# Performance work log

Measured on AMD Instinct MI355X. Metric: run time of the kernel, lower is better.

The kernel has to match this reference:

```python
import jax, jax.numpy as jnp
import numpy as np


def setup_inputs() -> dict:
    key = jax.random.key(0)
    k1, k2, k3, k4, k5 = jax.random.split(key, 5)
    B, D, H, W, C = 2, 16, 16, 16, 256
    x = jax.random.normal(k1, (B, D, H, W, C), dtype=jnp.float32)
    Wf = jax.random.normal(k2, (C, C // 4), dtype=jnp.float32) * (1.0 / np.sqrt(C))
    Wg = jax.random.normal(k3, (C, C // 4), dtype=jnp.float32) * (1.0 / np.sqrt(C))
    Wh = jax.random.normal(k4, (C, C), dtype=jnp.float32) * (1.0 / np.sqrt(C))
    gamma = jax.random.normal(k5, (1,), dtype=jnp.float32) * 0.1
    return {"x": x, "Wf": Wf, "Wg": Wg, "Wh": Wh, "gamma": gamma}


def reference(x, Wf, Wg, Wh, gamma):
    B, D, H, W, C = x.shape
    N = D * H * W
    xf = x.reshape(B, N, C)  # hw_flatten of input (1x1x1 conv == per-position matmul)
    f = jnp.einsum('bnc,cf->bnf', xf, Wf)   # [B, N, C//4]
    g = jnp.einsum('bnc,cf->bnf', xf, Wg)   # [B, N, C//4]
    h = jnp.einsum('bnc,cf->bnf', xf, Wh)   # [B, N, C]
    s = jnp.einsum('bnf,bmf->bnm', g, f)    # g @ f^T, [B, N, N]
    beta = jax.nn.softmax(s, axis=-1)
    o = jnp.einsum('bnm,bmc->bnc', beta, h)  # [B, N, C]
    out = gamma * o.reshape(B, D, H, W, C) + x
    beta_out = beta.reshape(-1, D, H, W, 1)  # [B*N, D, H, W, 1] as in original
    return (out, beta_out)
```

## Files before the change

### kernel.cpp

```cpp
#include <hip/hip_runtime.h>

#define NPOS 4096
#define CDIM 256
#define FDIM 64

typedef short short8 __attribute__((ext_vector_type(8)));
typedef float f32x4 __attribute__((ext_vector_type(4)));

__device__ __forceinline__ unsigned short f2bf(float v) {
  unsigned u = __float_as_uint(v);
  unsigned r = (u + 0x7fffu + ((u >> 16) & 1u)) >> 16;
  return (unsigned short)r;
}
__device__ __forceinline__ float bf2f(unsigned short u) {
  return __uint_as_float((unsigned)u << 16);
}
__device__ __forceinline__ short8 as_s8(uint4 u) {
  return *reinterpret_cast<short8*>(&u);
}
__device__ __forceinline__ void gload_lds16(const void* g, void* l) {
  __builtin_amdgcn_global_load_lds(
      (const __attribute__((address_space(1))) unsigned int*)g,
      (__attribute__((address_space(3))) unsigned int*)l, 16, 0, 0);
}

__global__ __launch_bounds__(256) void proj_kernel(
    const float* __restrict__ x, const float* __restrict__ Wf,
    const float* __restrict__ Wg, const float* __restrict__ Wh,
    unsigned short* __restrict__ f_hi, unsigned short* __restrict__ f_lo,
    unsigned short* __restrict__ g_hi, unsigned short* __restrict__ g_lo,
    unsigned short* __restrict__ h_t) {
  __shared__ float xs[16][CDIM];
  const int row0 = blockIdx.x * 16;
  const int t = threadIdx.x;
  {
    const float4* xv = reinterpret_cast<const float4*>(x + (size_t)row0 * CDIM);
    float4* sv = reinterpret_cast<float4*>(&xs[0][0]);
#pragma unroll
    for (int i = 0; i < 4; ++i) sv[t + 256 * i] = xv[t + 256 * i];
  }
  __syncthreads();
  {
    float acc[16];
#pragma unroll
    for (int r = 0; r < 16; ++r) acc[r] = 0.f;
    for (int k = 0; k < CDIM; k += 4) {
      const float w0 = Wh[(size_t)(k + 0) * CDIM + t];
      const float w1 = Wh[(size_t)(k + 1) * CDIM + t];
      const float w2 = Wh[(size_t)(k + 2) * CDIM + t];
      const float w3 = Wh[(size_t)(k + 3) * CDIM + t];
#pragma unroll
      for (int r = 0; r < 16; ++r) {
        const float4 xv = *reinterpret_cast<const float4*>(&xs[r][k]);
        float a = acc[r];
        a = fmaf(xv.x, w0, a);
        a = fmaf(xv.y, w1, a);
        a = fmaf(xv.z, w2, a);
        a = fmaf(xv.w, w3, a);
        acc[r] = a;
      }
    }
    const int b = row0 >> 12;
    const int lr = row0 & (NPOS - 1);
    unsigned wd[8];
#pragma unroll
    for (int i = 0; i < 8; ++i)
      wd[i] = (unsigned)f2bf(acc[2 * i]) | ((unsigned)f2bf(acc[2 * i + 1]) << 16);
    uint4* base = reinterpret_cast<uint4*>(h_t + ((size_t)(b * CDIM + t)) * NPOS);
    const int m = t & 7;
    const int c0 = lr >> 3;
    base[c0 ^ m] = make_uint4(wd[0], wd[1], wd[2], wd[3]);
    base[(c0 + 1) ^ m] = make_uint4(wd[4], wd[5], wd[6], wd[7]);
  }
  {
    const int col = t & 63;
    const int rb = (t >> 6) * 4;
    const int colq = col >> 3, cwi = col & 7;
    float af[4] = {0.f, 0.f, 0.f, 0.f};
    float ag[4] = {0.f, 0.f, 0.f, 0.f};
    for (int k = 0; k < CDIM; k += 4) {
      const float wf0 = Wf[(size_t)(k + 0) * FDIM + col];
      const float wf1 = Wf[(size_t)(k + 1) * FDIM + col];
      const float wf2 = Wf[(size_t)(k + 2) * FDIM + col];
      const float wf3 = Wf[(size_t)(k + 3) * FDIM + col];
      const float wg0 = Wg[(size_t)(k + 0) * FDIM + col];
      const float wg1 = Wg[(size_t)(k + 1) * FDIM + col];
      const float wg2 = Wg[(size_t)(k + 2) * FDIM + col];
      const float wg3 = Wg[(size_t)(k + 3) * FDIM + col];
#pragma unroll
      for (int r = 0; r < 4; ++r) {
        const float4 xv = *reinterpret_cast<const float4*>(&xs[rb + r][k]);
        float a = af[r], bb = ag[r];
        a = fmaf(xv.x, wf0, a); a = fmaf(xv.y, wf1, a);
        a = fmaf(xv.z, wf2, a); a = fmaf(xv.w, wf3, a);
        bb = fmaf(xv.x, wg0, bb); bb = fmaf(xv.y, wg1, bb);
        bb = fmaf(xv.z, wg2, bb); bb = fmaf(xv.w, wg3, bb);
        af[r] = a; ag[r] = bb;
      }
    }
#pragma unroll
    for (int r = 0; r < 4; ++r) {
      const int row = row0 + rb + r;
      const int ph = ((colq ^ (row & 7)) << 3) | cwi;
      const size_t of = (size_t)row * FDIM + ph;
      const size_t og = (size_t)row * FDIM + col;
      const unsigned short fh = f2bf(af[r]);
      const unsigned short gh = f2bf(ag[r]);
      f_hi[of] = fh;
      f_lo[of] = f2bf(af[r] - bf2f(fh));
      g_hi[og] = gh;
      g_lo[og] = f2bf(ag[r] - bf2f(gh));
    }
  }
}

__global__ __launch_bounds__(1024, 4) void attn_fused_kernel(
    const unsigned short* __restrict__ f_hi, const unsigned short* __restrict__ f_lo,
    const unsigned short* __restrict__ g_hi, const unsigned short* __restrict__ g_lo,
    const unsigned short* __restrict__ h_t, const float* __restrict__ x,
    const float* __restrict__ gamma, float* __restrict__ beta,
    float* __restrict__ out) {
  __shared__ __align__(16) char shraw[73728];
  __shared__ float partl[16][16];
  __shared__ float linvs[32];
  uint4 (*Fh)[128][8] = reinterpret_cast<uint4(*)[128][8]>(shraw);
  uint4 (*Fl)[128][8] = reinterpret_cast<uint4(*)[128][8]>(shraw + 32768);
  uint4 (*Ab)[32][8] = reinterpret_cast<uint4(*)[32][8]>(shraw);
  uint4 (*Bb)[256][8] = reinterpret_cast<uint4(*)[256][8]>(shraw + 8192);

  const int wg = blockIdx.x;
  const int wgid = (wg & 7) * 32 + (wg >> 3);
  const int b = wgid >> 7;
  const int row0 = (wgid & 127) * 32;
  const int t = threadIdx.x;
  const int w = t >> 6;
  const int l = t & 63;
  const int lr = l & 15;
  const int lk = l >> 4;

  const int wr = w >> 3;
  const int wq = w & 7;
  const int arow = row0 + wr * 16 + lr;
  short8 gh[2], gl[2];
  {
    const unsigned short* gH = g_hi + ((size_t)(b * NPOS + arow)) * FDIM + lk * 8;
    const unsigned short* gL = g_lo + ((size_t)(b * NPOS + arow)) * FDIM + lk * 8;
#pragma unroll
    for (int ks = 0; ks < 2; ++ks) {
      gh[ks] = *reinterpret_cast<const short8*>(gH + ks * 32);
      gl[ks] = *reinterpret_cast<const short8*>(gL + ks * 32);
    }
  }
  const unsigned short* fbh = f_hi + (size_t)b * NPOS * FDIM;
  const unsigned short* fbl = f_lo + (size_t)b * NPOS * FDIM;
  unsigned short* Pb = (unsigned short*)(beta + (size_t)b * NPOS * NPOS);
  unsigned short* prow = Pb + (size_t)arow * (2 * NPOS) + NPOS;
  const int rsw = lr & 7;
  float lsum = 0.f;
  const int srow_ = t >> 3, sch_ = t & 7;

#define STAGEA(buf, tile)                                                      \
  do {                                                                         \
    const int tr_ = (tile) * 128 + srow_;                                      \
    gload_lds16(fbh + (size_t)tr_ * FDIM + sch_ * 8,                           \
                (char*)&Fh[buf][0][0] + (size_t)t * 16);                       \
    gload_lds16(fbl + (size_t)tr_ * FDIM + sch_ * 8,                           \
                (char*)&Fl[buf][0][0] + (size_t)t * 16);                       \
  } while (0)

  STAGEA(0, 0);
  asm volatile("s_waitcnt vmcnt(0) lgkmcnt(0)\ns_barrier" ::: "memory");

  const int rrA = wq * 16 + lr;
  const int fsw = rrA & 7;
  int buf = 0;
  for (int tile = 0; tile < 32; ++tile) {
    if (tile < 31) STAGEA(buf ^ 1, tile + 1);
    __builtin_amdgcn_sched_barrier(0);
    const uint4 h0 = Fh[buf][rrA][lk ^ fsw];
    const uint4 h1 = Fh[buf][rrA][(lk + 4) ^ fsw];
    const uint4 q0 = Fl[buf][rrA][lk ^ fsw];
    const uint4 q1 = Fl[buf][rrA][(lk + 4) ^ fsw];
    f32x4 acca = {0.f, 0.f, 0.f, 0.f};
    f32x4 accb = {0.f, 0.f, 0.f, 0.f};
    acca = __builtin_amdgcn_mfma_f32_16x16x32_bf16(as_s8(h0), gh[0], acca, 0, 0, 0);
    accb = __builtin_amdgcn_mfma_f32_16x16x32_bf16(as_s8(h0), gl[0], accb, 0, 0, 0);
    acca = __builtin_amdgcn_mfma_f32_16x16x32_bf16(as_s8(q0), gh[0], acca, 0, 0, 0);
    accb = __builtin_amdgcn_mfma_f32_16x16x32_bf16(as_s8(h1), gh[1], accb, 0, 0, 0);
    acca = __builtin_amdgcn_mfma_f32_16x16x32_bf16(as_s8(q1), gh[1], acca, 0, 0, 0);
    accb = __builtin_amdgcn_mfma_f32_16x16x32_bf16(as_s8(h1), gl[1], accb, 0, 0, 0);
    const f32x4 acc = acca + accb;
    const int cq = tile * 128 + wq * 16 + lk * 4;
    const float e0 = __expf(acc[0]);
    const float e1 = __expf(acc[1]);
    const float e2 = __expf(acc[2]);
    const float e3 = __expf(acc[3]);
    lsum += (e0 + e1) + (e2 + e3);
    uint2 pk;
    pk.x = (unsigned)f2bf(e0) | ((unsigned)f2bf(e1) << 16);
    pk.y = (unsigned)f2bf(e2) | ((unsigned)f2bf(e3) << 16);
    const int sidx = (((cq >> 3) ^ rsw) << 3) | (cq & 7);
    *reinterpret_cast<uint2*>(prow + sidx) = pk;
    asm volatile("s_waitcnt vmcnt(1) lgkmcnt(0)\ns_barrier" ::: "memory");
    buf ^= 1;
  }
#undef STAGEA

  lsum += __shfl_xor(lsum, 16);
  lsum += __shfl_xor(lsum, 32);
  if (l < 16) partl[w][l] = lsum;
  __syncthreads();
  if (t < 32) {
    const int half = t >> 4;
    float s = 0.f;
#pragma unroll
    for (int q = 0; q < 8; ++q) s += partl[half * 8 + q][t & 15];
    linvs[t] = __frcp_rn(s);
  }
  asm volatile("s_waitcnt vmcnt(0) lgkmcnt(0)\ns_barrier" ::: "memory");

  const size_t hoff = (size_t)b * CDIM * NPOS;
  const unsigned short* Pub = (const unsigned short*)(beta + (size_t)b * NPOS * NPOS);

#define STAGEB(buf, kt)                                                         \
  do {                                                                          \
    {                                                                           \
      const int slot_ = w * 128 + l;                                            \
      const unsigned short* g_ = h_t + hoff + (size_t)(slot_ >> 3) * NPOS +     \
                                 (size_t)((kt) * 8 + (slot_ & 7)) * 8;          \
      gload_lds16(g_, (unsigned short*)&Bb[buf][0][0] + (size_t)(w * 128) * 8); \
    }                                                                           \
    {                                                                           \
      const int slot_ = w * 128 + 64 + l;                                       \
      const unsigned short* g_ = h_t + hoff + (size_t)(slot_ >> 3) * NPOS +     \
                                 (size_t)((kt) * 8 + (slot_ & 7)) * 8;          \
      gload_lds16(g_, (unsigned short*)&Bb[buf][0][0] +                         \
                          (size_t)(w * 128 + 64) * 8);                          \
    }                                                                           \
    if (t < 256) {                                                              \
      const unsigned short* g_ = Pub + (size_t)(row0 + (t >> 3)) * (2 * NPOS) + \
                                 NPOS + (size_t)((kt) * 8 + (t & 7)) * 8;       \
      gload_lds16(g_, (unsigned short*)&Ab[buf][0][0] + (size_t)(w * 64) * 8);  \
    }                                                                           \
  } while (0)

  f32x4 acc0 = {0.f, 0.f, 0.f, 0.f}, acc1 = {0.f, 0.f, 0.f, 0.f};
  const int wrB = w & 1;
  const int wcB = w >> 1;
  const int arB = wrB * 16 + lr;
  const int c0 = wcB * 32 + lr;
  const int c1 = c0 + 16;
  const int brow = t >> 5;
  const int jj = t & 31;

  STAGEB(0, 0);
  asm volatile("s_waitcnt vmcnt(0) lgkmcnt(0)\ns_barrier" ::: "memory");

  buf = 0;
  for (int kt = 0; kt < 64; ++kt) {
    if (kt < 63) STAGEB(buf ^ 1, kt + 1);
    __builtin_amdgcn_sched_barrier(0);
    {
      const uint4 a0 = Ab[buf][arB][lk ^ (arB & 7)];
      const uint4 a1 = Ab[buf][arB][(4 + lk) ^ (arB & 7)];
      const uint4 b00 = Bb[buf][c0][lk ^ (c0 & 7)];
      const uint4 b01 = Bb[buf][c1][lk ^ (c1 & 7)];
      const uint4 b10 = Bb[buf][c0][(4 + lk) ^ (c0 & 7)];
      const uint4 b11 = Bb[buf][c1][(4 + lk) ^ (c1 & 7)];
      acc0 = __builtin_amdgcn_mfma_f32_16x16x32_bf16(as_s8(a0), as_s8(b00), acc0, 0, 0, 0);
      acc1 = __builtin_amdgcn_mfma_f32_16x16x32_bf16(as_s8(a0), as_s8(b01), acc1, 0, 0, 0);
      acc0 = __builtin_amdgcn_mfma_f32_16x16x32_bf16(as_s8(a1), as_s8(b10), acc0, 0, 0, 0);
      acc1 = __builtin_amdgcn_mfma_f32_16x16x32_bf16(as_s8(a1), as_s8(b11), acc1, 0, 0, 0);
    }
    {
      const float il = linvs[brow];
      const unsigned* arow_ = reinterpret_cast<const unsigned*>(&Ab[buf][brow][0]);
      const unsigned u = arow_[(((jj >> 2) ^ (brow & 7)) << 2) | (jj & 3)];
      float2 v;
      v.x = bf2f((unsigned short)(u & 0xffffu)) * il;
      v.y = bf2f((unsigned short)(u >> 16)) * il;
      *reinterpret_cast<float2*>(beta + (size_t)(b * NPOS + row0 + brow) * NPOS +
                                 (size_t)kt * 64 + jj * 2) = v;
    }
    asm volatile("s_waitcnt vmcnt(1) lgkmcnt(0)\ns_barrier" ::: "memory");
    buf ^= 1;
  }
#undef STAGEB

  const float gam = gamma[0];
#pragma unroll
  for (int r = 0; r < 4; ++r) {
    const int lrr = wrB * 16 + lk * 4 + r;
    const int orow = row0 + lrr;
    const float sc = gam * linvs[lrr];
    const size_t i0 = ((size_t)b * NPOS + orow) * CDIM + wcB * 32 + lr;
    out[i0] = fmaf(sc, acc0[r], x[i0]);
    out[i0 + 16] = fmaf(sc, acc1[r], x[i0 + 16]);
  }
}

extern "C" void kernel_launch(void* const* d_in, const int* in_sizes, int n_in,
                              void* d_out, int out_size, void* d_ws, size_t ws_size,
                              hipStream_t stream) {
  (void)in_sizes; (void)n_in; (void)out_size; (void)ws_size;
  const float* x = (const float*)d_in[0];
  const float* Wf = (const float*)d_in[1];
  const float* Wg = (const float*)d_in[2];
  const float* Wh = (const float*)d_in[3];
  const float* gamma = (const float*)d_in[4];

  float* out = (float*)d_out;
  float* beta = out + (size_t)2 * NPOS * CDIM;

  unsigned short* h_t = (unsigned short*)d_ws;
  unsigned short* f_hi = h_t + (size_t)2 * CDIM * NPOS;
  unsigned short* f_lo = f_hi + (size_t)2 * NPOS * FDIM;
  unsigned short* g_hi = f_lo + (size_t)2 * NPOS * FDIM;
  unsigned short* g_lo = g_hi + (size_t)2 * NPOS * FDIM;

  hipLaunchKernelGGL(proj_kernel, dim3(2 * NPOS / 16), dim3(256), 0, stream,
                     x, Wf, Wg, Wh, f_hi, f_lo, g_hi, g_lo, h_t);
  hipLaunchKernelGGL(attn_fused_kernel, dim3(256), dim3(1024), 0, stream,
                     f_hi, f_lo, g_hi, g_lo, h_t, x, gamma, beta, out);
}
```

Before: 133.0 us.

## Halve rows per workgroup to launch 512 blocks of 512 threads

The fused attention kernel now handles 16 query rows per workgroup with 8 waves instead of 32 rows with 16 waves, doubling the grid to 512 workgroups. The staging loops, wave-to-tile mapping, LDS layout and the remapping of workgroups to batch and row are all adjusted to match. The aim is better spread across the MI355X compute units and less barrier cost per workgroup. In exchange, each F tile and each h tile staged into LDS now serves half as many rows, so global and LDS traffic per unit of work roughly doubles.

```diff
diff --git a/kernel.cpp b/kernel.cpp
--- a/kernel.cpp
+++ b/kernel.cpp
@@ -114,33 +114,31 @@
   }
 }
 
-__global__ __launch_bounds__(1024, 4) void attn_fused_kernel(
+__global__ __launch_bounds__(512, 4) void attn_fused_kernel(
     const unsigned short* __restrict__ f_hi, const unsigned short* __restrict__ f_lo,
     const unsigned short* __restrict__ g_hi, const unsigned short* __restrict__ g_lo,
     const unsigned short* __restrict__ h_t, const float* __restrict__ x,
     const float* __restrict__ gamma, float* __restrict__ beta,
     float* __restrict__ out) {
-  __shared__ __align__(16) char shraw[73728];
-  __shared__ float partl[16][16];
-  __shared__ float linvs[32];
+  __shared__ __align__(16) char shraw[69632];
+  __shared__ float partl[8][16];
+  __shared__ float linvs[16];
   uint4 (*Fh)[128][8] = reinterpret_cast<uint4(*)[128][8]>(shraw);
   uint4 (*Fl)[128][8] = reinterpret_cast<uint4(*)[128][8]>(shraw + 32768);
-  uint4 (*Ab)[32][8] = reinterpret_cast<uint4(*)[32][8]>(shraw);
-  uint4 (*Bb)[256][8] = reinterpret_cast<uint4(*)[256][8]>(shraw + 8192);
+  uint4 (*Ab)[16][8] = reinterpret_cast<uint4(*)[16][8]>(shraw);
+  uint4 (*Bb)[256][8] = reinterpret_cast<uint4(*)[256][8]>(shraw + 4096);
 
   const int wg = blockIdx.x;
-  const int wgid = (wg & 7) * 32 + (wg >> 3);
-  const int b = wgid >> 7;
-  const int row0 = (wgid & 127) * 32;
+  const int wgid = (wg & 7) * 64 + (wg >> 3);
+  const int b = wgid >> 8;
+  const int row0 = (wgid & 255) * 16;
   const int t = threadIdx.x;
   const int w = t >> 6;
   const int l = t & 63;
   const int lr = l & 15;
   const int lk = l >> 4;
 
-  const int wr = w >> 3;
-  const int wq = w & 7;
-  const int arow = row0 + wr * 16 + lr;
+  const int arow = row0 + lr;
   short8 gh[2], gl[2];
   {
     const unsigned short* gH = g_hi + ((size_t)(b * NPOS + arow)) * FDIM + lk * 8;
@@ -157,21 +155,25 @@
   unsigned short* prow = Pb + (size_t)arow * (2 * NPOS) + NPOS;
   const int rsw = lr & 7;
   float lsum = 0.f;
-  const int srow_ = t >> 3, sch_ = t & 7;
 
 #define STAGEA(buf, tile)                                                      \
   do {                                                                         \
-    const int tr_ = (tile) * 128 + srow_;                                      \
-    gload_lds16(fbh + (size_t)tr_ * FDIM + sch_ * 8,                           \
-                (char*)&Fh[buf][0][0] + (size_t)t * 16);                       \
-    gload_lds16(fbl + (size_t)tr_ * FDIM + sch_ * 8,                           \
-                (char*)&Fl[buf][0][0] + (size_t)t * 16);                       \
+    const int tile0_ = (tile) * 128;                                           \
+    _Pragma("unroll")                                                          \
+    for (int j = 0; j < 2; ++j) {                                              \
+      const int slot_ = j * 512 + t;                                           \
+      const int row_ = slot_ >> 3, ch_ = slot_ & 7;                            \
+      gload_lds16(fbh + (size_t)(tile0_ + row_) * FDIM + ch_ * 8,              \
+                  (char*)&Fh[buf][0][0] + (size_t)slot_ * 16);                 \
+      gload_lds16(fbl + (size_t)(tile0_ + row_) * FDIM + ch_ * 8,              \
+                  (char*)&Fl[buf][0][0] + (size_t)slot_ * 16);                 \
+    }                                                                          \
   } while (0)
 
   STAGEA(0, 0);
   asm volatile("s_waitcnt vmcnt(0) lgkmcnt(0)\ns_barrier" ::: "memory");
 
-  const int rrA = wq * 16 + lr;
+  const int rrA = w * 16 + lr;
   const int fsw = rrA & 7;
   int buf = 0;
   for (int tile = 0; tile < 32; ++tile) {
@@ -190,7 +192,7 @@
     acca = __builtin_amdgcn_mfma_f32_16x16x32_bf16(as_s8(q1), gh[1], acca, 0, 0, 0);
     accb = __builtin_amdgcn_mfma_f32_16x16x32_bf16(as_s8(h1), gl[1], accb, 0, 0, 0);
     const f32x4 acc = acca + accb;
-    const int cq = tile * 128 + wq * 16 + lk * 4;
+    const int cq = tile * 128 + w * 16 + lk * 4;
     const float e0 = __expf(acc[0]);
     const float e1 = __expf(acc[1]);
     const float e2 = __expf(acc[2]);
@@ -210,11 +212,10 @@
   lsum += __shfl_xor(lsum, 32);
   if (l < 16) partl[w][l] = lsum;
   __syncthreads();
-  if (t < 32) {
-    const int half = t >> 4;
+  if (t < 16) {
     float s = 0.f;
 #pragma unroll
-    for (int q = 0; q < 8; ++q) s += partl[half * 8 + q][t & 15];
+    for (int q = 0; q < 8; ++q) s += partl[q][t];
     linvs[t] = __frcp_rn(s);
   }
   asm volatile("s_waitcnt vmcnt(0) lgkmcnt(0)\ns_barrier" ::: "memory");
@@ -224,31 +225,22 @@
 
 #define STAGEB(buf, kt)                                                         \
   do {                                                                          \
-    {                                                                           \
-      const int slot_ = w * 128 + l;                                            \
+    _Pragma("unroll")                                                           \
+    for (int j = 0; j < 4; ++j) {                                               \
+      const int slot_ = j * 512 + t;                                            \
       const unsigned short* g_ = h_t + hoff + (size_t)(slot_ >> 3) * NPOS +     \
                                  (size_t)((kt) * 8 + (slot_ & 7)) * 8;          \
-      gload_lds16(g_, (unsigned short*)&Bb[buf][0][0] + (size_t)(w * 128) * 8); \
+      gload_lds16(g_, (char*)&Bb[buf][0][0] + (size_t)slot_ * 16);              \
     }                                                                           \
-    {                                                                           \
-      const int slot_ = w * 128 + 64 + l;                                       \
-      const unsigned short* g_ = h_t + hoff + (size_t)(slot_ >> 3) * NPOS +     \
-                                 (size_t)((kt) * 8 + (slot_ & 7)) * 8;          \
-      gload_lds16(g_, (unsigned short*)&Bb[buf][0][0] +                         \
-                          (size_t)(w * 128 + 64) * 8);                          \
-    }                                                                           \
-    if (t < 256) {                                                              \
+    if (t < 128) {                                                              \
       const unsigned short* g_ = Pub + (size_t)(row0 + (t >> 3)) * (2 * NPOS) + \
                                  NPOS + (size_t)((kt) * 8 + (t & 7)) * 8;       \
-      gload_lds16(g_, (unsigned short*)&Ab[buf][0][0] + (size_t)(w * 64) * 8);  \
+      gload_lds16(g_, (char*)&Ab[buf][0][0] + (size_t)t * 16);                  \
     }                                                                           \
   } while (0)
 
   f32x4 acc0 = {0.f, 0.f, 0.f, 0.f}, acc1 = {0.f, 0.f, 0.f, 0.f};
-  const int wrB = w & 1;
-  const int wcB = w >> 1;
-  const int arB = wrB * 16 + lr;
-  const int c0 = wcB * 32 + lr;
+  const int c0 = w * 32 + lr;
   const int c1 = c0 + 16;
   const int brow = t >> 5;
   const int jj = t & 31;
@@ -261,8 +253,8 @@
     if (kt < 63) STAGEB(buf ^ 1, kt + 1);
     __builtin_amdgcn_sched_barrier(0);
     {
-      const uint4 a0 = Ab[buf][arB][lk ^ (arB & 7)];
-      const uint4 a1 = Ab[buf][arB][(4 + lk) ^ (arB & 7)];
+      const uint4 a0 = Ab[buf][lr][lk ^ (lr & 7)];
+      const uint4 a1 = Ab[buf][lr][(4 + lk) ^ (lr & 7)];
       const uint4 b00 = Bb[buf][c0][lk ^ (c0 & 7)];
       const uint4 b01 = Bb[buf][c1][lk ^ (c1 & 7)];
       const uint4 b10 = Bb[buf][c0][(4 + lk) ^ (c0 & 7)];
@@ -290,10 +282,10 @@
   const float gam = gamma[0];
 #pragma unroll
   for (int r = 0; r < 4; ++r) {
-    const int lrr = wrB * 16 + lk * 4 + r;
+    const int lrr = lk * 4 + r;
     const int orow = row0 + lrr;
     const float sc = gam * linvs[lrr];
-    const size_t i0 = ((size_t)b * NPOS + orow) * CDIM + wcB * 32 + lr;
+    const size_t i0 = ((size_t)b * NPOS + orow) * CDIM + w * 32 + lr;
     out[i0] = fmaf(sc, acc0[r], x[i0]);
     out[i0 + 16] = fmaf(sc, acc1[r], x[i0 + 16]);
   }
@@ -320,6 +312,6 @@
 
   hipLaunchKernelGGL(proj_kernel, dim3(2 * NPOS / 16), dim3(256), 0, stream,
                      x, Wf, Wg, Wh, f_hi, f_lo, g_hi, g_lo, h_t);
-  hipLaunchKernelGGL(attn_fused_kernel, dim3(256), dim3(1024), 0, stream,
+  hipLaunchKernelGGL(attn_fused_kernel, dim3(512), dim3(512), 0, stream,
                      f_hi, f_lo, g_hi, g_lo, h_t, x, gamma, beta, out);
 }
```

After: 133.4 us. About the same (+0.3%).

## Split fused attention into QK/rowsum and split-K PV kernels with atomic accumulation

Applied to the files above, without the earlier changes.

Splits the fused attention kernel into two launches when the workspace is large enough. The first computes exp(QK) into a bf16 workspace plus row sums. The second runs P·V over 64-row tiles with the key dimension halved across workgroups, writes normalized beta, and atomically adds gamma-scaled partial outputs into out, which proj_kernel now pre-initializes with x. The aim is a better work shape per workgroup (64x256 output tiles with more MFMAs per LDS load), at the cost of an extra launch, a 64MB bf16 P round trip through memory, and float atomics. If the workspace is too small it falls back to the old fused kernel.

```diff
diff --git a/kernel.cpp b/kernel.cpp
--- a/kernel.cpp
+++ b/kernel.cpp
@@ -29,15 +29,20 @@
     const float* __restrict__ Wg, const float* __restrict__ Wh,
     unsigned short* __restrict__ f_hi, unsigned short* __restrict__ f_lo,
     unsigned short* __restrict__ g_hi, unsigned short* __restrict__ g_lo,
-    unsigned short* __restrict__ h_t) {
+    unsigned short* __restrict__ h_t, float* __restrict__ out) {
   __shared__ float xs[16][CDIM];
   const int row0 = blockIdx.x * 16;
   const int t = threadIdx.x;
   {
     const float4* xv = reinterpret_cast<const float4*>(x + (size_t)row0 * CDIM);
     float4* sv = reinterpret_cast<float4*>(&xs[0][0]);
-#pragma unroll
-    for (int i = 0; i < 4; ++i) sv[t + 256 * i] = xv[t + 256 * i];
+    float4* ov = reinterpret_cast<float4*>(out + (size_t)row0 * CDIM);
+#pragma unroll
+    for (int i = 0; i < 4; ++i) {
+      const float4 v = xv[t + 256 * i];
+      sv[t + 256 * i] = v;
+      ov[t + 256 * i] = v;
+    }
   }
   __syncthreads();
   {
@@ -114,19 +119,13 @@
   }
 }
 
-__global__ __launch_bounds__(1024, 4) void attn_fused_kernel(
+__global__ __launch_bounds__(1024, 4) void qk_l_kernel(
     const unsigned short* __restrict__ f_hi, const unsigned short* __restrict__ f_lo,
     const unsigned short* __restrict__ g_hi, const unsigned short* __restrict__ g_lo,
-    const unsigned short* __restrict__ h_t, const float* __restrict__ x,
-    const float* __restrict__ gamma, float* __restrict__ beta,
-    float* __restrict__ out) {
-  __shared__ __align__(16) char shraw[73728];
+    unsigned short* __restrict__ Pws, float* __restrict__ lrow) {
+  __shared__ uint4 Fh[2][128][8];
+  __shared__ uint4 Fl[2][128][8];
   __shared__ float partl[16][16];
-  __shared__ float linvs[32];
-  uint4 (*Fh)[128][8] = reinterpret_cast<uint4(*)[128][8]>(shraw);
-  uint4 (*Fl)[128][8] = reinterpret_cast<uint4(*)[128][8]>(shraw + 32768);
-  uint4 (*Ab)[32][8] = reinterpret_cast<uint4(*)[32][8]>(shraw);
-  uint4 (*Bb)[256][8] = reinterpret_cast<uint4(*)[256][8]>(shraw + 8192);
 
   const int wg = blockIdx.x;
   const int wgid = (wg & 7) * 32 + (wg >> 3);
@@ -153,8 +152,7 @@
   }
   const unsigned short* fbh = f_hi + (size_t)b * NPOS * FDIM;
   const unsigned short* fbl = f_lo + (size_t)b * NPOS * FDIM;
-  unsigned short* Pb = (unsigned short*)(beta + (size_t)b * NPOS * NPOS);
-  unsigned short* prow = Pb + (size_t)arow * (2 * NPOS) + NPOS;
+  unsigned short* prow = Pws + (size_t)(b * NPOS + arow) * NPOS;
   const int rsw = lr & 7;
   float lsum = 0.f;
   const int srow_ = t >> 3, sch_ = t & 7;
@@ -215,6 +213,224 @@
     float s = 0.f;
 #pragma unroll
     for (int q = 0; q < 8; ++q) s += partl[half * 8 + q][t & 15];
+    lrow[(size_t)b * NPOS + row0 + t] = s;
+  }
+}
+
+__global__ __launch_bounds__(1024, 4) void pv_split_kernel(
+    const unsigned short* __restrict__ h_t, const unsigned short* __restrict__ Pws,
+    const float* __restrict__ lrow, const float* __restrict__ gamma,
+    float* __restrict__ beta, float* __restrict__ out) {
+  __shared__ uint4 Ab[2][64][8];
+  __shared__ uint4 Bb[2][256][8];
+  __shared__ float linvB[64];
+
+  const int wg = blockIdx.x;
+  const int wgid = (wg & 7) * 32 + (wg >> 3);
+  const int b = wgid >> 7;
+  const int khalf = (wgid >> 6) & 1;
+  const int row0 = (wgid & 63) * 64;
+  const int t = threadIdx.x;
+  const int w = t >> 6;
+  const int l = t & 63;
+  const int lr = l & 15;
+  const int lk = l >> 4;
+
+  if (t < 64) linvB[t] = __frcp_rn(lrow[(size_t)b * NPOS + row0 + t]);
+
+  const size_t hoff = (size_t)b * CDIM * NPOS;
+  const unsigned short* Pb = Pws + (size_t)(b * NPOS + row0) * NPOS;
+  const int kbase = khalf * 256;
+
+#define STAGEB(bufi, kt)                                                        \
+  do {                                                                          \
+    _Pragma("unroll")                                                           \
+    for (int j = 0; j < 2; ++j) {                                               \
+      const int slot_ = j * 1024 + t;                                           \
+      const int col_ = slot_ >> 3, ch_ = slot_ & 7;                             \
+      const unsigned short* g_ = h_t + hoff + (size_t)col_ * NPOS +             \
+                                 (size_t)(kbase + (kt) * 8 + ch_) * 8;          \
+      gload_lds16(g_, (char*)&Bb[bufi][0][0] + (size_t)slot_ * 16);             \
+    }                                                                           \
+    if (t < 512) {                                                              \
+      const int row_ = t >> 3, ch_ = t & 7;                                     \
+      const unsigned short* g_ = Pb + (size_t)row_ * NPOS +                     \
+                                 (size_t)(kbase + (kt) * 8 + ch_) * 8;          \
+      gload_lds16(g_, (char*)&Ab[bufi][0][0] + (size_t)t * 16);                 \
+    }                                                                           \
+  } while (0)
+
+  f32x4 acc0 = {0.f, 0.f, 0.f, 0.f}, acc1 = {0.f, 0.f, 0.f, 0.f};
+  f32x4 acc2 = {0.f, 0.f, 0.f, 0.f}, acc3 = {0.f, 0.f, 0.f, 0.f};
+  const int wrB = w & 3;
+  const int wcB = w >> 2;
+  const int arB = wrB * 16 + lr;
+  const int c0 = wcB * 64 + lr;
+  const int c1 = c0 + 16;
+  const int c2 = c0 + 32;
+  const int c3 = c0 + 48;
+  const int brow = t >> 4;
+  const int jj = t & 15;
+
+  STAGEB(0, 0);
+  asm volatile("s_waitcnt vmcnt(0) lgkmcnt(0)\ns_barrier" ::: "memory");
+  const float il_brow = linvB[brow];
+
+  int buf = 0;
+  for (int kt = 0; kt < 32; ++kt) {
+    if (kt < 31) STAGEB(buf ^ 1, kt + 1);
+    __builtin_amdgcn_sched_barrier(0);
+    {
+      const uint4 a0 = Ab[buf][arB][lk ^ (arB & 7)];
+      const uint4 a1 = Ab[buf][arB][(4 + lk) ^ (arB & 7)];
+      const uint4 b00 = Bb[buf][c0][lk ^ (c0 & 7)];
+      const uint4 b01 = Bb[buf][c1][lk ^ (c1 & 7)];
+      const uint4 b02 = Bb[buf][c2][lk ^ (c2 & 7)];
+      const uint4 b03 = Bb[buf][c3][lk ^ (c3 & 7)];
+      acc0 = __builtin_amdgcn_mfma_f32_16x16x32_bf16(as_s8(a0), as_s8(b00), acc0, 0, 0, 0);
+      acc1 = __builtin_amdgcn_mfma_f32_16x16x32_bf16(as_s8(a0), as_s8(b01), acc1, 0, 0, 0);
+      acc2 = __builtin_amdgcn_mfma_f32_16x16x32_bf16(as_s8(a0), as_s8(b02), acc2, 0, 0, 0);
+      acc3 = __builtin_amdgcn_mfma_f32_16x16x32_bf16(as_s8(a0), as_s8(b03), acc3, 0, 0, 0);
+      const uint4 b10 = Bb[buf][c0][(4 + lk) ^ (c0 & 7)];
+      const uint4 b11 = Bb[buf][c1][(4 + lk) ^ (c1 & 7)];
+      const uint4 b12 = Bb[buf][c2][(4 + lk) ^ (c2 & 7)];
+      const uint4 b13 = Bb[buf][c3][(4 + lk) ^ (c3 & 7)];
+      acc0 = __builtin_amdgcn_mfma_f32_16x16x32_bf16(as_s8(a1), as_s8(b10), acc0, 0, 0, 0);
+      acc1 = __builtin_amdgcn_mfma_f32_16x16x32_bf16(as_s8(a1), as_s8(b11), acc1, 0, 0, 0);
+      acc2 = __builtin_amdgcn_mfma_f32_16x16x32_bf16(as_s8(a1), as_s8(b12), acc2, 0, 0, 0);
+      acc3 = __builtin_amdgcn_mfma_f32_16x16x32_bf16(as_s8(a1), as_s8(b13), acc3, 0, 0, 0);
+    }
+    {
+      const uint4 u4 = Ab[buf][brow][(jj >> 1) ^ (brow & 7)];
+      const uint2 u = (jj & 1) ? make_uint2(u4.z, u4.w) : make_uint2(u4.x, u4.y);
+      float4 v;
+      v.x = bf2f((unsigned short)(u.x & 0xffffu)) * il_brow;
+      v.y = bf2f((unsigned short)(u.x >> 16)) * il_brow;
+      v.z = bf2f((unsigned short)(u.y & 0xffffu)) * il_brow;
+      v.w = bf2f((unsigned short)(u.y >> 16)) * il_brow;
+      *reinterpret_cast<float4*>(beta + (size_t)(b * NPOS + row0 + brow) * NPOS +
+                                 khalf * 2048 + kt * 64 + jj * 4) = v;
+    }
+    asm volatile("s_waitcnt vmcnt(1) lgkmcnt(0)\ns_barrier" ::: "memory");
+    buf ^= 1;
+  }
+#undef STAGEB
+
+  const float gam = gamma[0];
+#pragma unroll
+  for (int r = 0; r < 4; ++r) {
+    const int lrr = wrB * 16 + lk * 4 + r;
+    const int orow = row0 + lrr;
+    const float sc = gam * linvB[lrr];
+    float* o = out + ((size_t)b * NPOS + orow) * CDIM + wcB * 64 + lr;
+    atomicAdd(o, sc * acc0[r]);
+    atomicAdd(o + 16, sc * acc1[r]);
+    atomicAdd(o + 32, sc * acc2[r]);
+    atomicAdd(o + 48, sc * acc3[r]);
+  }
+}
+
+__global__ __launch_bounds__(1024, 4) void attn_fused_kernel(
+    const unsigned short* __restrict__ f_hi, const unsigned short* __restrict__ f_lo,
+    const unsigned short* __restrict__ g_hi, const unsigned short* __restrict__ g_lo,
+    const unsigned short* __restrict__ h_t, const float* __restrict__ x,
+    const float* __restrict__ gamma, float* __restrict__ beta,
+    float* __restrict__ out) {
+  __shared__ __align__(16) char shraw[110592];
+  __shared__ float partl[16][16];
+  __shared__ float linvs[32];
+  uint4 (*Fh)[128][8] = reinterpret_cast<uint4(*)[128][8]>(shraw);
+  uint4 (*Fl)[128][8] = reinterpret_cast<uint4(*)[128][8]>(shraw + 32768);
+  uint4 (*Ab)[32][8] = reinterpret_cast<uint4(*)[32][8]>(shraw);
+  uint4 (*Bb)[256][8] = reinterpret_cast<uint4(*)[256][8]>(shraw + 12288);
+
+  const int wg = blockIdx.x;
+  const int wgid = (wg & 7) * 32 + (wg >> 3);
+  const int b = wgid >> 7;
+  const int row0 = (wgid & 127) * 32;
+  const int t = threadIdx.x;
+  const int w = t >> 6;
+  const int l = t & 63;
+  const int lr = l & 15;
+  const int lk = l >> 4;
+
+  const int wr = w >> 3;
+  const int wq = w & 7;
+  const int arow = row0 + wr * 16 + lr;
+  short8 gh[2], gl[2];
+  {
+    const unsigned short* gH = g_hi + ((size_t)(b * NPOS + arow)) * FDIM + lk * 8;
+    const unsigned short* gL = g_lo + ((size_t)(b * NPOS + arow)) * FDIM + lk * 8;
+#pragma unroll
+    for (int ks = 0; ks < 2; ++ks) {
+      gh[ks] = *reinterpret_cast<const short8*>(gH + ks * 32);
+      gl[ks] = *reinterpret_cast<const short8*>(gL + ks * 32);
+    }
+  }
+  const unsigned short* fbh = f_hi + (size_t)b * NPOS * FDIM;
+  const unsigned short* fbl = f_lo + (size_t)b * NPOS * FDIM;
+  unsigned short* Pb = (unsigned short*)(beta + (size_t)b * NPOS * NPOS);
+  unsigned short* prow = Pb + (size_t)arow * (2 * NPOS) + NPOS;
+  const int rsw = lr & 7;
+  float lsum = 0.f;
+  const int srow_ = t >> 3, sch_ = t & 7;
+
+#define STAGEA(buf, tile)                                                      \
+  do {                                                                         \
+    const int tr_ = (tile) * 128 + srow_;                                      \
+    gload_lds16(fbh + (size_t)tr_ * FDIM + sch_ * 8,                           \
+                (char*)&Fh[buf][0][0] + (size_t)t * 16);                       \
+    gload_lds16(fbl + (size_t)tr_ * FDIM + sch_ * 8,                           \
+                (char*)&Fl[buf][0][0] + (size_t)t * 16);                       \
+  } while (0)
+
+  STAGEA(0, 0);
+  asm volatile("s_waitcnt vmcnt(0) lgkmcnt(0)\ns_barrier" ::: "memory");
+
+  const int rrA = wq * 16 + lr;
+  const int fsw = rrA & 7;
+  int buf = 0;
+  for (int tile = 0; tile < 32; ++tile) {
+    if (tile < 31) STAGEA(buf ^ 1, tile + 1);
+    __builtin_amdgcn_sched_barrier(0);
+    const uint4 h0 = Fh[buf][rrA][lk ^ fsw];
+    const uint4 h1 = Fh[buf][rrA][(lk + 4) ^ fsw];
+    const uint4 q0 = Fl[buf][rrA][lk ^ fsw];
+    const uint4 q1 = Fl[buf][rrA][(lk + 4) ^ fsw];
+    f32x4 acca = {0.f, 0.f, 0.f, 0.f};
+    f32x4 accb = {0.f, 0.f, 0.f, 0.f};
+    acca = __builtin_amdgcn_mfma_f32_16x16x32_bf16(as_s8(h0), gh[0], acca, 0, 0, 0);
+    accb = __builtin_amdgcn_mfma_f32_16x16x32_bf16(as_s8(h0), gl[0], accb, 0, 0, 0);
+    acca = __builtin_amdgcn_mfma_f32_16x16x32_bf16(as_s8(q0), gh[0], acca, 0, 0, 0);
+    accb = __builtin_amdgcn_mfma_f32_16x16x32_bf16(as_s8(h1), gh[1], accb, 0, 0, 0);
+    acca = __builtin_amdgcn_mfma_f32_16x16x32_bf16(as_s8(q1), gh[1], acca, 0, 0, 0);
+    accb = __builtin_amdgcn_mfma_f32_16x16x32_bf16(as_s8(h1), gl[1], accb, 0, 0, 0);
+    const f32x4 acc = acca + accb;
+    const int cq = tile * 128 + wq * 16 + lk * 4;
+    const float e0 = __expf(acc[0]);
+    const float e1 = __expf(acc[1]);
+    const float e2 = __expf(acc[2]);
+    const float e3 = __expf(acc[3]);
+    lsum += (e0 + e1) + (e2 + e3);
+    uint2 pk;
+    pk.x = (unsigned)f2bf(e0) | ((unsigned)f2bf(e1) << 16);
+    pk.y = (unsigned)f2bf(e2) | ((unsigned)f2bf(e3) << 16);
+    const int sidx = (((cq >> 3) ^ rsw) << 3) | (cq & 7);
+    *reinterpret_cast<uint2*>(prow + sidx) = pk;
+    asm volatile("s_waitcnt vmcnt(1) lgkmcnt(0)\ns_barrier" ::: "memory");
+    buf ^= 1;
+  }
+#undef STAGEA
+
+  lsum += __shfl_xor(lsum, 16);
+  lsum += __shfl_xor(lsum, 32);
+  if (l < 16) partl[w][l] = lsum;
+  __syncthreads();
+  if (t < 32) {
+    const int half = t >> 4;
+    float s = 0.f;
+#pragma unroll
+    for (int q = 0; q < 8; ++q) s += partl[half * 8 + q][t & 15];
     linvs[t] = __frcp_rn(s);
   }
   asm volatile("s_waitcnt vmcnt(0) lgkmcnt(0)\ns_barrier" ::: "memory");
@@ -222,25 +438,25 @@
   const size_t hoff = (size_t)b * CDIM * NPOS;
   const unsigned short* Pub = (const unsigned short*)(beta + (size_t)b * NPOS * NPOS);
 
-#define STAGEB(buf, kt)                                                         \
+#define STAGEB(bufi, kt)                                                        \
   do {                                                                          \
     {                                                                           \
       const int slot_ = w * 128 + l;                                            \
       const unsigned short* g_ = h_t + hoff + (size_t)(slot_ >> 3) * NPOS +     \
                                  (size_t)((kt) * 8 + (slot_ & 7)) * 8;          \
-      gload_lds16(g_, (unsigned short*)&Bb[buf][0][0] + (size_t)(w * 128) * 8); \
+      gload_lds16(g_, (unsigned short*)&Bb[bufi][0][0] + (size_t)(w * 128) * 8);\
     }                                                                           \
     {                                                                           \
       const int slot_ = w * 128 + 64 + l;                                       \
       const unsigned short* g_ = h_t + hoff + (size_t)(slot_ >> 3) * NPOS +     \
                                  (size_t)((kt) * 8 + (slot_ & 7)) * 8;          \
-      gload_lds16(g_, (unsigned short*)&Bb[buf][0][0] +                         \
+      gload_lds16(g_, (unsigned short*)&Bb[bufi][0][0] +                        \
                           (size_t)(w * 128 + 64) * 8);                          \
     }                                                                           \
     if (t < 256) {                                                              \
       const unsigned short* g_ = Pub + (size_t)(row0 + (t >> 3)) * (2 * NPOS) + \
                                  NPOS + (size_t)((kt) * 8 + (t & 7)) * 8;       \
-      gload_lds16(g_, (unsigned short*)&Ab[buf][0][0] + (size_t)(w * 64) * 8);  \
+      gload_lds16(g_, (unsigned short*)&Ab[bufi][0][0] + (size_t)(w * 64) * 8); \
     }                                                                           \
   } while (0)
 
@@ -252,6 +468,7 @@
   const int c1 = c0 + 16;
   const int brow = t >> 5;
   const int jj = t & 31;
+  const float il_brow = linvs[brow];
 
   STAGEB(0, 0);
   asm volatile("s_waitcnt vmcnt(0) lgkmcnt(0)\ns_barrier" ::: "memory");
@@ -273,12 +490,11 @@
       acc1 = __builtin_amdgcn_mfma_f32_16x16x32_bf16(as_s8(a1), as_s8(b11), acc1, 0, 0, 0);
     }
     {
-      const float il = linvs[brow];
       const unsigned* arow_ = reinterpret_cast<const unsigned*>(&Ab[buf][brow][0]);
       const unsigned u = arow_[(((jj >> 2) ^ (brow & 7)) << 2) | (jj & 3)];
       float2 v;
-      v.x = bf2f((unsigned short)(u & 0xffffu)) * il;
-      v.y = bf2f((unsigned short)(u >> 16)) * il;
+      v.x = bf2f((unsigned short)(u & 0xffffu)) * il_brow;
+      v.y = bf2f((unsigned short)(u >> 16)) * il_brow;
       *reinterpret_cast<float2*>(beta + (size_t)(b * NPOS + row0 + brow) * NPOS +
                                  (size_t)kt * 64 + jj * 2) = v;
     }
@@ -302,7 +518,7 @@
 extern "C" void kernel_launch(void* const* d_in, const int* in_sizes, int n_in,
                               void* d_out, int out_size, void* d_ws, size_t ws_size,
                               hipStream_t stream) {
-  (void)in_sizes; (void)n_in; (void)out_size; (void)ws_size;
+  (void)in_sizes; (void)n_in; (void)out_size;
   const float* x = (const float*)d_in[0];
   const float* Wf = (const float*)d_in[1];
   const float* Wg = (const float*)d_in[2];
@@ -317,9 +533,20 @@
   unsigned short* f_lo = f_hi + (size_t)2 * NPOS * FDIM;
   unsigned short* g_hi = f_lo + (size_t)2 * NPOS * FDIM;
   unsigned short* g_lo = g_hi + (size_t)2 * NPOS * FDIM;
+  float* lrow = (float*)(g_lo + (size_t)2 * NPOS * FDIM);
+  unsigned short* Pws = (unsigned short*)(lrow + 2 * NPOS);
+
+  const size_t need = ((char*)(Pws + (size_t)2 * NPOS * NPOS)) - (char*)d_ws;
 
   hipLaunchKernelGGL(proj_kernel, dim3(2 * NPOS / 16), dim3(256), 0, stream,
-                     x, Wf, Wg, Wh, f_hi, f_lo, g_hi, g_lo, h_t);
-  hipLaunchKernelGGL(attn_fused_kernel, dim3(256), dim3(1024), 0, stream,
-                     f_hi, f_lo, g_hi, g_lo, h_t, x, gamma, beta, out);
-}
+                     x, Wf, Wg, Wh, f_hi, f_lo, g_hi, g_lo, h_t, out);
+  if (ws_size >= need) {
+    hipLaunchKernelGGL(qk_l_kernel, dim3(256), dim3(1024), 0, stream,
+                       f_hi, f_lo, g_hi, g_lo, Pws, lrow);
+    hipLaunchKernelGGL(pv_split_kernel, dim3(256), dim3(1024), 0, stream,
+                       h_t, Pws, lrow, gamma, beta, out);
+  } else {
+    hipLaunchKernelGGL(attn_fused_kernel, dim3(256), dim3(1024), 0, stream,
+                       f_hi, f_lo, g_hi, g_lo, h_t, x, gamma, beta, out);
+  }
+}
```

Measured after the change: 131.0 us. Within noise of the previous version (-1.5%).
